# Kernel tuning notes

Hardware: AMD Instinct MI355X
Metric: run time of the kernel (lower is better)

The kernel has to match this reference:

```python
import jax, jax.numpy as jnp
import numpy as np

B, S, D = 16, 2048, 128

def setup_inputs() -> dict:
    key = jax.random.key(0)
    kq, kk, kv = jax.random.split(key, 3)
    return {
        "query": jax.random.normal(kq, (B, S, D), dtype=jnp.float32),
        "key": jax.random.normal(kk, (B, S, D), dtype=jnp.float32),
        "value": jax.random.normal(kv, (B, S, D), dtype=jnp.float32),
    }

def reference(query, key, value):
    # query: (B, S2, d), key: (B, S1, d), value: (B, S1, d)
    d_k = query.shape[-1]
    scale = 1.0 / jnp.sqrt(jnp.asarray(d_k, dtype=query.dtype))
    # (B, S2, S1) attention scores
    att = jnp.einsum('bqd,bkd->bqk', query, key) * scale
    att = jax.nn.softmax(att, axis=-1)
    # (B, S2, d_v)
    return jnp.einsum('bqk,bkd->bqd', att, value)
```

## Files before the change

### kernel.cpp

```cpp
#include <hip/hip_runtime.h>

#define B_N 16
#define S_LEN 2048
#define D_DIM 128
#define TK 32
#define NTH 32

typedef __attribute__((ext_vector_type(16))) float f32x16;
typedef __attribute__((ext_vector_type(8)))  short short8;
typedef __attribute__((ext_vector_type(4)))  int   i32x4;
typedef const __attribute__((address_space(1))) void* gp1;
typedef __attribute__((address_space(3))) void* sp3;
#define GLL(g, l) __builtin_amdgcn_global_load_lds((gp1)(const void*)(g), (sp3)(void*)(l), 16, 0, 0)

static __device__ __forceinline__ unsigned short f2bf(float f) {
  unsigned u = __builtin_bit_cast(unsigned, f);
  return (unsigned short)((u + 0x7fffu + ((u >> 16) & 1u)) >> 16);
}

__global__ __launch_bounds__(256)
void prep_kernel(const float* __restrict__ K, const float* __restrict__ V,
                 unsigned short* __restrict__ Kb, unsigned short* __restrict__ VT) {
  __shared__ unsigned short lds[64 * 66];
  int bx = blockIdx.x;
  int t  = threadIdx.x;
  if (bx < 4096) {
    size_t i = ((size_t)bx * 256 + t) * 4;
    float4 v = *(const float4*)(K + i);
    unsigned lo = (unsigned)f2bf(v.x) | ((unsigned)f2bf(v.y) << 16);
    unsigned hi = (unsigned)f2bf(v.z) | ((unsigned)f2bf(v.w) << 16);
    *(uint2*)(Kb + i) = make_uint2(lo, hi);
  } else {
    int bi = bx - 4096;
    int b  = bi & 15;
    int st = (bi >> 4) & 31;
    int dt = bi >> 9;
    const float* Vb = V + ((size_t)b * S_LEN + st * 64) * D_DIM + dt * 64;
    unsigned short* VTb = VT + ((size_t)b * D_DIM + dt * 64) * S_LEN + st * 64;
#pragma unroll
    for (int rep = 0; rep < 4; ++rep) {
      int idx = rep * 256 + t;
      int i  = idx >> 4;
      int j4 = (idx & 15) * 4;
      float4 v = *(const float4*)(Vb + (size_t)i * D_DIM + j4);
      unsigned lo = (unsigned)f2bf(v.x) | ((unsigned)f2bf(v.y) << 16);
      unsigned hi = (unsigned)f2bf(v.z) | ((unsigned)f2bf(v.w) << 16);
      *(uint2*)&lds[i * 66 + j4] = make_uint2(lo, hi);
    }
    __syncthreads();
#pragma unroll
    for (int rep = 0; rep < 4; ++rep) {
      int idx = rep * 256 + t;
      int dd = idx >> 4;
      int s4 = (idx & 15) * 4;
      unsigned short e0 = lds[(s4 + 0) * 66 + dd];
      unsigned short e1 = lds[(s4 + 1) * 66 + dd];
      unsigned short e2 = lds[(s4 + 2) * 66 + dd];
      unsigned short e3 = lds[(s4 + 3) * 66 + dd];
      *(uint2*)(VTb + (size_t)dd * S_LEN + s4) =
          make_uint2((unsigned)e0 | ((unsigned)e1 << 16),
                     (unsigned)e2 | ((unsigned)e3 << 16));
    }
  }
}

__global__ __launch_bounds__(512, 2)
void attn_kernel(const float* __restrict__ Q, const unsigned short* __restrict__ Kb,
                 const unsigned short* __restrict__ VT, float* __restrict__ O) {
  __shared__ __align__(16) char smem[98304];

  const int tid  = threadIdx.x;
  const int wave = tid >> 6;
  const int g    = wave >> 2;
  const int w4   = wave & 3;
  const int lane = tid & 63;
  const int l32  = lane & 31;
  const int half = lane >> 5;

  const int i     = blockIdx.x;
  const int b     = (i & 7) * 2 + ((i >> 3) & 1);
  const int qtile = i >> 4;
  const int qbase = qtile * 128 + w4 * 32;

  const float* Qb = Q + (size_t)b * S_LEN * D_DIM;
  const unsigned short* Kbb = Kb + (size_t)b * S_LEN * D_DIM;
  const unsigned short* VTb = VT + (size_t)b * D_DIM * S_LEN;

  unsigned short* kb0 = (unsigned short*)smem + (size_t)g * 3 * 4096;
  unsigned short* vb0 = (unsigned short*)(smem + 49152) + (size_t)g * 3 * 4096;

#define ISSUE_TILE(tt, buf)                                                        \
  {                                                                                \
    const int T_ = g * NTH + (tt);                                                 \
    _Pragma("unroll")                                                              \
    for (int cc = 0; cc < 2; ++cc) {                                               \
      int c = w4 * 2 + cc;                                                         \
      int rl = 4 * c + (lane >> 4);                                                \
      int lbk = (lane & 15) ^ (rl & 15);                                           \
      GLL(Kbb + (size_t)(T_ * TK + rl) * D_DIM + lbk * 8, kb0 + (buf) * 4096 + c * 512); \
      int dv = 16 * c + (lane >> 2);                                               \
      int lbv = (lane & 3) ^ ((dv >> 1) & 3);                                      \
      GLL(VTb + (size_t)dv * S_LEN + T_ * TK + lbv * 8, vb0 + (buf) * 4096 + c * 512);   \
    }                                                                              \
  }

  ISSUE_TILE(0, 0)
  ISSUE_TILE(1, 1)

  short8 qa[8];
  {
    const float* qp = Qb + (size_t)(qbase + l32) * D_DIM + half * 8;
#pragma unroll
    for (int ks = 0; ks < 8; ++ks) {
      float4 a0 = *(const float4*)(qp + ks * 16);
      float4 a1 = *(const float4*)(qp + ks * 16 + 4);
      short8 f;
      f[0] = (short)f2bf(a0.x); f[1] = (short)f2bf(a0.y);
      f[2] = (short)f2bf(a0.z); f[3] = (short)f2bf(a0.w);
      f[4] = (short)f2bf(a1.x); f[5] = (short)f2bf(a1.y);
      f[6] = (short)f2bf(a1.z); f[7] = (short)f2bf(a1.w);
      qa[ks] = f;
    }
  }

  const f32x16 zf16 = {0.f,0.f,0.f,0.f,0.f,0.f,0.f,0.f,0.f,0.f,0.f,0.f,0.f,0.f,0.f,0.f};
  f32x16 oacc[4];
  float lsum = 0.f;
#pragma unroll
  for (int dt = 0; dt < 4; ++dt) oacc[dt] = zf16;

  const float SC = 0.08838834764831845f * 1.4426950408889634f;

  int cur = 0;
  int pre = 2;
  for (int t = 0; t < NTH; ++t) {
    if (t + 1 < NTH) {
      asm volatile("s_waitcnt vmcnt(4)" ::: "memory");
    } else {
      asm volatile("s_waitcnt vmcnt(0)" ::: "memory");
    }
    __builtin_amdgcn_s_barrier();

    if (t + 2 < NTH) ISSUE_TILE(t + 2, pre)

    const unsigned short* kbc = kb0 + cur * 4096;
    const unsigned short* vbc = vb0 + cur * 4096;

    f32x16 sacc = zf16;
#pragma unroll
    for (int ks = 0; ks < 8; ++ks) {
      int pk = (ks * 2 + half) ^ (l32 & 15);
      short8 kf = *(const short8*)&kbc[l32 * D_DIM + pk * 8];
      sacc = __builtin_amdgcn_mfma_f32_32x32x16_bf16(kf, qa[ks], sacc, 0, 0, 0);
    }

    float p[16];
#pragma unroll
    for (int reg = 0; reg < 16; ++reg) {
      p[reg] = exp2f(sacc[reg] * SC);
      lsum += p[reg];
    }

    int dw[8];
#pragma unroll
    for (int i2 = 0; i2 < 8; ++i2)
      asm("v_cvt_pk_bf16_f32 %0, %1, %2"
          : "=v"(dw[i2]) : "v"(p[2 * i2]), "v"(p[2 * i2 + 1]));
    asm("v_permlane32_swap_b32 %0, %1" : "+v"(dw[0]), "+v"(dw[2]));
    asm("v_permlane32_swap_b32 %0, %1" : "+v"(dw[1]), "+v"(dw[3]));
    asm("v_permlane32_swap_b32 %0, %1" : "+v"(dw[4]), "+v"(dw[6]));
    asm("v_permlane32_swap_b32 %0, %1" : "+v"(dw[5]), "+v"(dw[7]));
    i32x4 f0 = {dw[0], dw[1], dw[2], dw[3]};
    i32x4 f1 = {dw[4], dw[5], dw[6], dw[7]};
    short8 pf[2];
    pf[0] = __builtin_bit_cast(short8, f0);
    pf[1] = __builtin_bit_cast(short8, f1);

#pragma unroll
    for (int ks2 = 0; ks2 < 2; ++ks2) {
#pragma unroll
      for (int dt = 0; dt < 4; ++dt) {
        int dv = dt * 32 + l32;
        int pv = (ks2 * 2 + half) ^ ((dv >> 1) & 3);
        short8 vf = *(const short8*)&vbc[dv * TK + pv * 8];
        oacc[dt] = __builtin_amdgcn_mfma_f32_32x32x16_bf16(pf[ks2], vf, oacc[dt], 0, 0, 0);
      }
    }

    cur = (cur == 2) ? 0 : cur + 1;
    pre = (pre == 2) ? 0 : pre + 1;
  }
#undef ISSUE_TILE

  lsum += __shfl_xor(lsum, 32);

  __syncthreads();
  float* mo  = (float*)(smem + w4 * 16640);
  float* ml1 = (float*)(smem + w4 * 16640 + 16384);
  float* ml0 = ml1 + 32;
  if (g == 1) {
#pragma unroll
    for (int reg = 0; reg < 16; ++reg) {
      int row = (reg & 3) + 8 * (reg >> 2) + 4 * half;
#pragma unroll
      for (int dt = 0; dt < 4; ++dt)
        mo[row * 128 + dt * 32 + l32] = oacc[dt][reg];
    }
    if (half == 0) ml1[l32] = lsum;
  } else {
    if (half == 0) ml0[l32] = lsum;
  }
  __syncthreads();
  if (g == 0) {
    float* Ob = O + (size_t)b * S_LEN * D_DIM;
#pragma unroll
    for (int reg = 0; reg < 16; ++reg) {
      int row = (reg & 3) + 8 * (reg >> 2) + 4 * half;
      float linv = 1.f / (ml0[row] + ml1[row]);
#pragma unroll
      for (int dt = 0; dt < 4; ++dt)
        Ob[(size_t)(qbase + row) * D_DIM + dt * 32 + l32] =
            (oacc[dt][reg] + mo[row * 128 + dt * 32 + l32]) * linv;
    }
  }
}

extern "C" void kernel_launch(void* const* d_in, const int* in_sizes, int n_in,
                              void* d_out, int out_size, void* d_ws, size_t ws_size,
                              hipStream_t stream) {
  const float* Q = (const float*)d_in[0];
  const float* K = (const float*)d_in[1];
  const float* V = (const float*)d_in[2];
  float* O = (float*)d_out;
  unsigned short* Kb = (unsigned short*)d_ws;
  unsigned short* VT = Kb + (size_t)B_N * S_LEN * D_DIM;
  prep_kernel<<<dim3(4096 + 1024), dim3(256), 0, stream>>>(K, V, Kb, VT);
  attn_kernel<<<dim3(256), dim3(512), 0, stream>>>(Q, Kb, VT, O);
}
```

Baseline: 137.3 us.

## Software-pipeline QK and PV across tiles with 4-deep LDS ring and setprio

```diff
diff --git a/kernel.cpp b/kernel.cpp
--- a/kernel.cpp
+++ b/kernel.cpp
@@ -24,14 +24,17 @@
   __shared__ unsigned short lds[64 * 66];
   int bx = blockIdx.x;
   int t  = threadIdx.x;
-  if (bx < 4096) {
-    size_t i = ((size_t)bx * 256 + t) * 4;
-    float4 v = *(const float4*)(K + i);
-    unsigned lo = (unsigned)f2bf(v.x) | ((unsigned)f2bf(v.y) << 16);
-    unsigned hi = (unsigned)f2bf(v.z) | ((unsigned)f2bf(v.w) << 16);
-    *(uint2*)(Kb + i) = make_uint2(lo, hi);
+  if (bx < 1024) {
+#pragma unroll
+    for (int rep = 0; rep < 4; ++rep) {
+      size_t i = (((size_t)rep * 1024 + bx) * 256 + t) * 4;
+      float4 v = *(const float4*)(K + i);
+      unsigned lo = (unsigned)f2bf(v.x) | ((unsigned)f2bf(v.y) << 16);
+      unsigned hi = (unsigned)f2bf(v.z) | ((unsigned)f2bf(v.w) << 16);
+      *(uint2*)(Kb + i) = make_uint2(lo, hi);
+    }
   } else {
-    int bi = bx - 4096;
+    int bi = bx - 1024;
     int b  = bi & 15;
     int st = (bi >> 4) & 31;
     int dt = bi >> 9;
@@ -67,7 +70,7 @@
 __global__ __launch_bounds__(512, 2)
 void attn_kernel(const float* __restrict__ Q, const unsigned short* __restrict__ Kb,
                  const unsigned short* __restrict__ VT, float* __restrict__ O) {
-  __shared__ __align__(16) char smem[98304];
+  __shared__ __align__(16) char smem[131072];
 
   const int tid  = threadIdx.x;
   const int wave = tid >> 6;
@@ -86,8 +89,8 @@
   const unsigned short* Kbb = Kb + (size_t)b * S_LEN * D_DIM;
   const unsigned short* VTb = VT + (size_t)b * D_DIM * S_LEN;
 
-  unsigned short* kb0 = (unsigned short*)smem + (size_t)g * 3 * 4096;
-  unsigned short* vb0 = (unsigned short*)(smem + 49152) + (size_t)g * 3 * 4096;
+  unsigned short* kb0 = (unsigned short*)smem + (size_t)g * 4 * 4096;
+  unsigned short* vb0 = (unsigned short*)(smem + 65536) + (size_t)g * 4 * 4096;
 
 #define ISSUE_TILE(tt, buf)                                                        \
   {                                                                                \
@@ -104,8 +107,58 @@
     }                                                                              \
   }
 
-  ISSUE_TILE(0, 0)
-  ISSUE_TILE(1, 1)
+#define QK_TILE(buf, saccv)                                                        \
+  {                                                                                \
+    const unsigned short* kbc_ = kb0 + (buf) * 4096;                               \
+    __builtin_amdgcn_s_setprio(1);                                                 \
+    _Pragma("unroll")                                                              \
+    for (int ks = 0; ks < 8; ++ks) {                                               \
+      int pk = (ks * 2 + half) ^ (l32 & 15);                                       \
+      short8 kf = *(const short8*)&kbc_[l32 * D_DIM + pk * 8];                     \
+      saccv = __builtin_amdgcn_mfma_f32_32x32x16_bf16(kf, qa[ks], saccv, 0, 0, 0); \
+    }                                                                              \
+    __builtin_amdgcn_s_setprio(0);                                                 \
+  }
+
+#define SOFTMAX(saccv, pf0v, pf1v)                                                 \
+  {                                                                                \
+    float p_[16];                                                                  \
+    _Pragma("unroll")                                                              \
+    for (int reg = 0; reg < 16; ++reg) {                                           \
+      p_[reg] = exp2f(saccv[reg] * SC);                                            \
+      lsum += p_[reg];                                                             \
+    }                                                                              \
+    int dw_[8];                                                                    \
+    _Pragma("unroll")                                                              \
+    for (int i2 = 0; i2 < 8; ++i2)                                                 \
+      asm("v_cvt_pk_bf16_f32 %0, %1, %2"                                           \
+          : "=v"(dw_[i2]) : "v"(p_[2 * i2]), "v"(p_[2 * i2 + 1]));                 \
+    asm("v_permlane32_swap_b32 %0, %1" : "+v"(dw_[0]), "+v"(dw_[2]));              \
+    asm("v_permlane32_swap_b32 %0, %1" : "+v"(dw_[1]), "+v"(dw_[3]));              \
+    asm("v_permlane32_swap_b32 %0, %1" : "+v"(dw_[4]), "+v"(dw_[6]));              \
+    asm("v_permlane32_swap_b32 %0, %1" : "+v"(dw_[5]), "+v"(dw_[7]));              \
+    i32x4 f0_ = {dw_[0], dw_[1], dw_[2], dw_[3]};                                  \
+    i32x4 f1_ = {dw_[4], dw_[5], dw_[6], dw_[7]};                                  \
+    pf0v = __builtin_bit_cast(short8, f0_);                                        \
+    pf1v = __builtin_bit_cast(short8, f1_);                                        \
+  }
+
+#define PV_TILE(buf, pf0v, pf1v)                                                   \
+  {                                                                                \
+    const unsigned short* vbc_ = vb0 + (buf) * 4096;                               \
+    __builtin_amdgcn_s_setprio(1);                                                 \
+    _Pragma("unroll")                                                              \
+    for (int dt = 0; dt < 4; ++dt) {                                               \
+      int dv = dt * 32 + l32;                                                      \
+      int pv0 = half ^ ((dv >> 1) & 3);                                            \
+      short8 vf0 = *(const short8*)&vbc_[dv * TK + pv0 * 8];                       \
+      oacc[dt] = __builtin_amdgcn_mfma_f32_32x32x16_bf16(pf0v, vf0, oacc[dt], 0, 0, 0); \
+      int pv1 = (2 + half) ^ ((dv >> 1) & 3);                                      \
+      short8 vf1 = *(const short8*)&vbc_[dv * TK + pv1 * 8];                       \
+      oacc[dt] = __builtin_amdgcn_mfma_f32_32x32x16_bf16(pf1v, vf1, oacc[dt], 0, 0, 0); \
+    }                                                                              \
+    __builtin_amdgcn_s_setprio(0);                                                 \
+  }
 
   short8 qa[8];
   {
@@ -123,6 +176,10 @@
     }
   }
 
+  ISSUE_TILE(0, 0)
+  ISSUE_TILE(1, 1)
+  ISSUE_TILE(2, 2)
+
   const f32x16 zf16 = {0.f,0.f,0.f,0.f,0.f,0.f,0.f,0.f,0.f,0.f,0.f,0.f,0.f,0.f,0.f,0.f};
   f32x16 oacc[4];
   float lsum = 0.f;
@@ -131,66 +188,44 @@
 
   const float SC = 0.08838834764831845f * 1.4426950408889634f;
 
-  int cur = 0;
-  int pre = 2;
-  for (int t = 0; t < NTH; ++t) {
-    if (t + 1 < NTH) {
-      asm volatile("s_waitcnt vmcnt(4)" ::: "memory");
-    } else {
-      asm volatile("s_waitcnt vmcnt(0)" ::: "memory");
-    }
+  f32x16 saccA = zf16, saccB;
+  short8 pfA0, pfA1, pfB0, pfB1;
+
+  asm volatile("s_waitcnt vmcnt(8)" ::: "memory");
+  __builtin_amdgcn_s_barrier();
+  QK_TILE(0, saccA)
+
+  for (int t = 0; t + 3 < NTH; t += 2) {
+    SOFTMAX(saccA, pfA0, pfA1)
+    asm volatile("s_waitcnt vmcnt(4)" ::: "memory");
     __builtin_amdgcn_s_barrier();
-
-    if (t + 2 < NTH) ISSUE_TILE(t + 2, pre)
-
-    const unsigned short* kbc = kb0 + cur * 4096;
-    const unsigned short* vbc = vb0 + cur * 4096;
-
-    f32x16 sacc = zf16;
-#pragma unroll
-    for (int ks = 0; ks < 8; ++ks) {
-      int pk = (ks * 2 + half) ^ (l32 & 15);
-      short8 kf = *(const short8*)&kbc[l32 * D_DIM + pk * 8];
-      sacc = __builtin_amdgcn_mfma_f32_32x32x16_bf16(kf, qa[ks], sacc, 0, 0, 0);
-    }
-
-    float p[16];
-#pragma unroll
-    for (int reg = 0; reg < 16; ++reg) {
-      p[reg] = exp2f(sacc[reg] * SC);
-      lsum += p[reg];
-    }
-
-    int dw[8];
-#pragma unroll
-    for (int i2 = 0; i2 < 8; ++i2)
-      asm("v_cvt_pk_bf16_f32 %0, %1, %2"
-          : "=v"(dw[i2]) : "v"(p[2 * i2]), "v"(p[2 * i2 + 1]));
-    asm("v_permlane32_swap_b32 %0, %1" : "+v"(dw[0]), "+v"(dw[2]));
-    asm("v_permlane32_swap_b32 %0, %1" : "+v"(dw[1]), "+v"(dw[3]));
-    asm("v_permlane32_swap_b32 %0, %1" : "+v"(dw[4]), "+v"(dw[6]));
-    asm("v_permlane32_swap_b32 %0, %1" : "+v"(dw[5]), "+v"(dw[7]));
-    i32x4 f0 = {dw[0], dw[1], dw[2], dw[3]};
-    i32x4 f1 = {dw[4], dw[5], dw[6], dw[7]};
-    short8 pf[2];
-    pf[0] = __builtin_bit_cast(short8, f0);
-    pf[1] = __builtin_bit_cast(short8, f1);
-
-#pragma unroll
-    for (int ks2 = 0; ks2 < 2; ++ks2) {
-#pragma unroll
-      for (int dt = 0; dt < 4; ++dt) {
-        int dv = dt * 32 + l32;
-        int pv = (ks2 * 2 + half) ^ ((dv >> 1) & 3);
-        short8 vf = *(const short8*)&vbc[dv * TK + pv * 8];
-        oacc[dt] = __builtin_amdgcn_mfma_f32_32x32x16_bf16(pf[ks2], vf, oacc[dt], 0, 0, 0);
-      }
-    }
-
-    cur = (cur == 2) ? 0 : cur + 1;
-    pre = (pre == 2) ? 0 : pre + 1;
-  }
+    ISSUE_TILE(t + 3, (t + 3) & 3)
+    saccB = zf16;
+    QK_TILE((t + 1) & 3, saccB)
+    PV_TILE(t & 3, pfA0, pfA1)
+
+    SOFTMAX(saccB, pfB0, pfB1)
+    asm volatile("s_waitcnt vmcnt(4)" ::: "memory");
+    __builtin_amdgcn_s_barrier();
+    if (t + 4 < NTH) ISSUE_TILE(t + 4, (t + 4) & 3)
+    saccA = zf16;
+    QK_TILE((t + 2) & 3, saccA)
+    PV_TILE((t + 1) & 3, pfB0, pfB1)
+  }
+
+  SOFTMAX(saccA, pfA0, pfA1)
+  asm volatile("s_waitcnt vmcnt(0)" ::: "memory");
+  __builtin_amdgcn_s_barrier();
+  saccB = zf16;
+  QK_TILE(31 & 3, saccB)
+  PV_TILE(30 & 3, pfA0, pfA1)
+  SOFTMAX(saccB, pfB0, pfB1)
+  PV_TILE(31 & 3, pfB0, pfB1)
+
 #undef ISSUE_TILE
+#undef QK_TILE
+#undef SOFTMAX
+#undef PV_TILE
 
   lsum += __shfl_xor(lsum, 32);
 
@@ -234,6 +269,6 @@
   float* O = (float*)d_out;
   unsigned short* Kb = (unsigned short*)d_ws;
   unsigned short* VT = Kb + (size_t)B_N * S_LEN * D_DIM;
-  prep_kernel<<<dim3(4096 + 1024), dim3(256), 0, stream>>>(K, V, Kb, VT);
+  prep_kernel<<<dim3(1024 + 1024), dim3(256), 0, stream>>>(K, V, Kb, VT);
   attn_kernel<<<dim3(256), dim3(512), 0, stream>>>(Q, Kb, VT, O);
 }
```

Result: no change. 138.6 us (median of 2 runs) (+0.9%).

## Halve attention block size, split K/V prefetch with double-buffered V

Applied to the files above, without the earlier changes.

```diff
diff --git a/kernel.cpp b/kernel.cpp
--- a/kernel.cpp
+++ b/kernel.cpp
@@ -24,14 +24,17 @@
   __shared__ unsigned short lds[64 * 66];
   int bx = blockIdx.x;
   int t  = threadIdx.x;
-  if (bx < 4096) {
-    size_t i = ((size_t)bx * 256 + t) * 4;
-    float4 v = *(const float4*)(K + i);
-    unsigned lo = (unsigned)f2bf(v.x) | ((unsigned)f2bf(v.y) << 16);
-    unsigned hi = (unsigned)f2bf(v.z) | ((unsigned)f2bf(v.w) << 16);
-    *(uint2*)(Kb + i) = make_uint2(lo, hi);
+  if (bx < 1024) {
+#pragma unroll
+    for (int rep = 0; rep < 4; ++rep) {
+      size_t i = (((size_t)rep * 1024 + bx) * 256 + t) * 4;
+      float4 v = *(const float4*)(K + i);
+      unsigned lo = (unsigned)f2bf(v.x) | ((unsigned)f2bf(v.y) << 16);
+      unsigned hi = (unsigned)f2bf(v.z) | ((unsigned)f2bf(v.w) << 16);
+      *(uint2*)(Kb + i) = make_uint2(lo, hi);
+    }
   } else {
-    int bi = bx - 4096;
+    int bi = bx - 1024;
     int b  = bi & 15;
     int st = (bi >> 4) & 31;
     int dt = bi >> 9;
@@ -64,15 +67,15 @@
   }
 }
 
-__global__ __launch_bounds__(512, 2)
+__global__ __launch_bounds__(256, 2)
 void attn_kernel(const float* __restrict__ Q, const unsigned short* __restrict__ Kb,
                  const unsigned short* __restrict__ VT, float* __restrict__ O) {
-  __shared__ __align__(16) char smem[98304];
+  __shared__ __align__(16) char smem[81920];
 
   const int tid  = threadIdx.x;
   const int wave = tid >> 6;
-  const int g    = wave >> 2;
-  const int w4   = wave & 3;
+  const int g    = wave >> 1;
+  const int w4   = wave & 1;
   const int lane = tid & 63;
   const int l32  = lane & 31;
   const int half = lane >> 5;
@@ -80,32 +83,37 @@
   const int i     = blockIdx.x;
   const int b     = (i & 7) * 2 + ((i >> 3) & 1);
   const int qtile = i >> 4;
-  const int qbase = qtile * 128 + w4 * 32;
+  const int qbase = qtile * 64 + w4 * 32;
 
   const float* Qb = Q + (size_t)b * S_LEN * D_DIM;
   const unsigned short* Kbb = Kb + (size_t)b * S_LEN * D_DIM;
   const unsigned short* VTb = VT + (size_t)b * D_DIM * S_LEN;
 
   unsigned short* kb0 = (unsigned short*)smem + (size_t)g * 3 * 4096;
-  unsigned short* vb0 = (unsigned short*)(smem + 49152) + (size_t)g * 3 * 4096;
-
-#define ISSUE_TILE(tt, buf)                                                        \
+  unsigned short* vb0 = (unsigned short*)(smem + 49152) + (size_t)g * 2 * 4096;
+
+#define ISSUE_K(tt, buf)                                                           \
   {                                                                                \
     const int T_ = g * NTH + (tt);                                                 \
     _Pragma("unroll")                                                              \
-    for (int cc = 0; cc < 2; ++cc) {                                               \
-      int c = w4 * 2 + cc;                                                         \
+    for (int cc = 0; cc < 4; ++cc) {                                               \
+      int c = w4 * 4 + cc;                                                         \
       int rl = 4 * c + (lane >> 4);                                                \
       int lbk = (lane & 15) ^ (rl & 15);                                           \
       GLL(Kbb + (size_t)(T_ * TK + rl) * D_DIM + lbk * 8, kb0 + (buf) * 4096 + c * 512); \
+    }                                                                              \
+  }
+#define ISSUE_V(tt, buf)                                                           \
+  {                                                                                \
+    const int T_ = g * NTH + (tt);                                                 \
+    _Pragma("unroll")                                                              \
+    for (int cc = 0; cc < 4; ++cc) {                                               \
+      int c = w4 * 4 + cc;                                                         \
       int dv = 16 * c + (lane >> 2);                                               \
       int lbv = (lane & 3) ^ ((dv >> 1) & 3);                                      \
       GLL(VTb + (size_t)dv * S_LEN + T_ * TK + lbv * 8, vb0 + (buf) * 4096 + c * 512);   \
     }                                                                              \
   }
-
-  ISSUE_TILE(0, 0)
-  ISSUE_TILE(1, 1)
 
   short8 qa[8];
   {
@@ -123,6 +131,10 @@
     }
   }
 
+  ISSUE_K(0, 0)
+  ISSUE_V(0, 0)
+  ISSUE_K(1, 1)
+
   const f32x16 zf16 = {0.f,0.f,0.f,0.f,0.f,0.f,0.f,0.f,0.f,0.f,0.f,0.f,0.f,0.f,0.f,0.f};
   f32x16 oacc[4];
   float lsum = 0.f;
@@ -131,8 +143,9 @@
 
   const float SC = 0.08838834764831845f * 1.4426950408889634f;
 
-  int cur = 0;
-  int pre = 2;
+  int kcur = 0;
+  int kpre = 2;
+  int vcur = 0;
   for (int t = 0; t < NTH; ++t) {
     if (t + 1 < NTH) {
       asm volatile("s_waitcnt vmcnt(4)" ::: "memory");
@@ -141,10 +154,11 @@
     }
     __builtin_amdgcn_s_barrier();
 
-    if (t + 2 < NTH) ISSUE_TILE(t + 2, pre)
-
-    const unsigned short* kbc = kb0 + cur * 4096;
-    const unsigned short* vbc = vb0 + cur * 4096;
+    if (t + 1 < NTH) ISSUE_V(t + 1, vcur ^ 1)
+    if (t + 2 < NTH) ISSUE_K(t + 2, kpre)
+
+    const unsigned short* kbc = kb0 + kcur * 4096;
+    const unsigned short* vbc = vb0 + vcur * 4096;
 
     f32x16 sacc = zf16;
 #pragma unroll
@@ -187,10 +201,12 @@
       }
     }
 
-    cur = (cur == 2) ? 0 : cur + 1;
-    pre = (pre == 2) ? 0 : pre + 1;
-  }
-#undef ISSUE_TILE
+    kcur = (kcur == 2) ? 0 : kcur + 1;
+    kpre = (kpre == 2) ? 0 : kpre + 1;
+    vcur ^= 1;
+  }
+#undef ISSUE_K
+#undef ISSUE_V
 
   lsum += __shfl_xor(lsum, 32);
 
@@ -234,6 +250,6 @@
   float* O = (float*)d_out;
   unsigned short* Kb = (unsigned short*)d_ws;
   unsigned short* VT = Kb + (size_t)B_N * S_LEN * D_DIM;
-  prep_kernel<<<dim3(4096 + 1024), dim3(256), 0, stream>>>(K, V, Kb, VT);
-  attn_kernel<<<dim3(256), dim3(512), 0, stream>>>(Q, Kb, VT, O);
-}
+  prep_kernel<<<dim3(1024 + 1024), dim3(256), 0, stream>>>(K, V, Kb, VT);
+  attn_kernel<<<dim3(512), dim3(256), 0, stream>>>(Q, Kb, VT, O);
+}
```

Result: slower. 141.2 us (+2.8%).
